# Kernel optimization log

Measured on AMD Instinct MI355X. Metric: run time of the kernel, lower is better.

## Reference

```python
import jax, jax.numpy as jnp
import numpy as np

N_NODES = 100000
N_EDGES = 1600000
IN_F = 512
OUT_F = 128


def setup_inputs() -> dict:
    key = jax.random.key(0)
    k1, k2, k3, k4, k5 = jax.random.split(key, 5)
    x = jax.random.normal(k1, (N_NODES, IN_F), dtype=jnp.float32)
    adj_row = jnp.sort(jax.random.randint(k2, (N_EDGES,), 0, N_NODES, dtype=jnp.int32))
    adj_col = jax.random.randint(k3, (N_EDGES,), 0, N_NODES, dtype=jnp.int32)
    adj_vals = jax.random.uniform(k4, (N_EDGES,), dtype=jnp.float32)
    # Xavier-uniform init like nn.init.xavier_uniform_
    limit = float(np.sqrt(6.0 / (IN_F + OUT_F)))
    weight = jax.random.uniform(k5, (IN_F, OUT_F), minval=-limit, maxval=limit, dtype=jnp.float32)
    return {"x": x, "adj_row": adj_row, "adj_col": adj_col, "adj_vals": adj_vals, "weight": weight}


def reference(x, adj_row, adj_col, adj_vals, weight):
    # support = input @ weight  (dense GEMM; torch.spmm with dense-equivalent input)
    support = x @ weight                      # [N, OUT_F]
    # output = adj @ support, adj in COO: gather cols, scale, segment-sum by row
    msgs = adj_vals[:, None] * support[adj_col]          # [E, OUT_F]
    output = jax.ops.segment_sum(msgs, adj_row, num_segments=N_NODES)  # [N, OUT_F]
    return output
```

## Files before the change

### kernel.cpp

```cpp
#include <hip/hip_runtime.h>
#include <hip/hip_bf16.h>

typedef __bf16 bf16;
typedef __attribute__((ext_vector_type(8))) __bf16 bf16x8;
typedef __attribute__((ext_vector_type(4))) __bf16 bf16x4;
typedef __attribute__((ext_vector_type(2))) __bf16 bf16x2;
typedef __attribute__((ext_vector_type(4))) float f32x4;

#define IN_F 512
#define OUT_F 128
#define BM 64
#define BK 64
#define NKT (IN_F / BK)
#define RPB 32
#define PAGE 512
#define UNR 16

__global__ __launch_bounds__(256) void wt_convert_kernel(const float* __restrict__ w,
                                                         bf16* __restrict__ wt_frag) {
    int o = blockIdx.x * 256 + threadIdx.x;
    int e   = o & 7;
    int l   = (o >> 3) & 63;
    int nb  = (o >> 9) & 7;
    int kkt = o >> 12;
    int n = nb * 16 + (l & 15);
    int k = (kkt >> 1) * 64 + (kkt & 1) * 32 + (l >> 4) * 8 + e;
    wt_frag[o] = (bf16)w[k * OUT_F + n];
}

__global__ __launch_bounds__(256) void row_ptr_kernel(const int* __restrict__ adj_row,
                                                      int* __restrict__ row_ptr,
                                                      int n_edges, int n_nodes) {
    int e = blockIdx.x * 256 + threadIdx.x;
    if (e >= n_edges) return;
    int r1 = adj_row[e];
    int r0 = (e == 0) ? -1 : adj_row[e - 1];
    for (int r = r0 + 1; r <= r1; ++r) row_ptr[r] = e;
    if (e == n_edges - 1)
        for (int r = r1 + 1; r <= n_nodes; ++r) row_ptr[r] = n_edges;
}

__global__ __launch_bounds__(256) void gemm_kernel(const float* __restrict__ x,
                                                   const bf16* __restrict__ wt_frag,
                                                   bf16* __restrict__ support,
                                                   int n_nodes) {
    __shared__ bf16 As[2][BM * BK];

    const int tid  = threadIdx.x;
    const int lane = tid & 63;
    const int wid  = tid >> 6;
    const int row0 = blockIdx.x * BM;

    float4 av[4];

    auto load_tile = [&](int kt) {
        const int k0 = kt * BK;
        #pragma unroll
        for (int i = 0; i < 4; ++i) {
            int li = i * 256 + tid;
            int r = li >> 4, c4 = li & 15;
            int grow = row0 + r;
            float4 v = {0.f, 0.f, 0.f, 0.f};
            if (grow < n_nodes)
                v = *reinterpret_cast<const float4*>(x + (size_t)grow * IN_F + k0 + c4 * 4);
            av[i] = v;
        }
    };

    auto write_tile = [&](int buf) {
        char* Ab = (char*)As[buf];
        #pragma unroll
        for (int i = 0; i < 4; ++i) {
            int li = i * 256 + tid;
            int r = li >> 4, c4 = li & 15;
            bf16x4 b;
            b[0] = (bf16)av[i].x; b[1] = (bf16)av[i].y;
            b[2] = (bf16)av[i].z; b[3] = (bf16)av[i].w;
            *reinterpret_cast<bf16x4*>(Ab + ((r * 128 + c4 * 8) ^ ((r & 7) << 4))) = b;
        }
    };

    load_tile(0);
    write_tile(0);
    __syncthreads();

    f32x4 acc[4][2] = {};

    for (int kt = 0; kt < NKT; ++kt) {
        const int cur = kt & 1;

        bf16x8 b[2][2];
        #pragma unroll
        for (int kk = 0; kk < 2; ++kk)
            #pragma unroll
            for (int n = 0; n < 2; ++n) {
                int f = (kt * 2 + kk) * 8 + (wid * 2 + n);
                b[kk][n] = *reinterpret_cast<const bf16x8*>(wt_frag + ((size_t)f * 64 + lane) * 8);
            }

        if (kt < NKT - 1) load_tile(kt + 1);

        const char* Ab = (const char*)As[cur];
        #pragma unroll
        for (int kk = 0; kk < 2; ++kk) {
            const int kbyte = kk * 64 + (lane >> 4) * 16;
            bf16x8 a[4];
            #pragma unroll
            for (int m = 0; m < 4; ++m) {
                int r = m * 16 + (lane & 15);
                a[m] = *reinterpret_cast<const bf16x8*>(Ab + ((r * 128 + kbyte) ^ ((r & 7) << 4)));
            }
            #pragma unroll
            for (int m = 0; m < 4; ++m)
                #pragma unroll
                for (int n = 0; n < 2; ++n)
                    acc[m][n] = __builtin_amdgcn_mfma_f32_16x16x32_bf16(a[m], b[kk][n], acc[m][n], 0, 0, 0);
        }

        if (kt < NKT - 1) {
            write_tile(cur ^ 1);
            __syncthreads();
        }
    }

    #pragma unroll
    for (int m = 0; m < 4; ++m) {
        #pragma unroll
        for (int n = 0; n < 2; ++n) {
            #pragma unroll
            for (int j = 0; j < 4; ++j) {
                int gm = row0 + m * 16 + (lane >> 4) * 4 + j;
                int gn = wid * 32 + n * 16 + (lane & 15);
                if (gm < n_nodes)
                    support[(size_t)gm * OUT_F + gn] = (bf16)acc[m][n][j];
            }
        }
    }
}

__global__ __launch_bounds__(64) void scatter_kernel(const int* __restrict__ adj_row,
                                                     const int* __restrict__ adj_col,
                                                     const float* __restrict__ adj_vals,
                                                     const bf16* __restrict__ support,
                                                     const int* __restrict__ row_ptr,
                                                     float* __restrict__ out,
                                                     int n_nodes) {
    __shared__ int   srow[PAGE];
    __shared__ int   scol[PAGE];
    __shared__ float sval[PAGE];

    const int t    = threadIdx.x;
    const int r0   = blockIdx.x * RPB;
    const int rEnd = min(r0 + RPB, n_nodes);
    const int eLo  = row_ptr[r0];
    const int eHi  = row_ptr[rEnd];

    float accx = 0.f, accy = 0.f;
    int   cur  = r0;

    auto flush_to = [&](int rNew) {
        if (cur < rEnd) {
            float2 st = {accx, accy};
            *reinterpret_cast<float2*>(out + (size_t)cur * OUT_F + t * 2) = st;
        }
        float2 z = {0.f, 0.f};
        int zhi = rNew < rEnd ? rNew : rEnd;
        for (int r = cur + 1; r < zhi; ++r)
            *reinterpret_cast<float2*>(out + (size_t)r * OUT_F + t * 2) = z;
        accx = 0.f; accy = 0.f;
        cur = rNew;
    };

    for (int base = eLo; base < eHi; base += PAGE) {
        const int nE = min(PAGE, eHi - base);
        __syncthreads();
        for (int i = t; i < nE; i += 64) {
            srow[i] = adj_row[base + i];
            scol[i] = adj_col[base + i];
            sval[i] = adj_vals[base + i];
        }
        __syncthreads();
        if (nE < PAGE) {
            for (int i = nE + t; i < PAGE; i += 64) {
                srow[i] = n_nodes;
                scol[i] = 0;
                sval[i] = 0.f;
            }
            __syncthreads();
        }

        for (int i0 = 0; i0 < PAGE; i0 += UNR) {
            if (i0 >= nE) break;
            float mx[UNR], my[UNR];
            #pragma unroll
            for (int u = 0; u < UNR; ++u) {
                int   c = scol[i0 + u];
                float s = sval[i0 + u];
                bf16x2 v = *reinterpret_cast<const bf16x2*>(support + (size_t)c * OUT_F + t * 2);
                mx[u] = s * (float)v[0];
                my[u] = s * (float)v[1];
            }
            #pragma unroll
            for (int u = 0; u < UNR; ++u) {
                int r = srow[i0 + u];
                if (r != cur) flush_to(r);
                accx += mx[u]; accy += my[u];
            }
        }
    }
    flush_to(rEnd);
}

extern "C" void kernel_launch(void* const* d_in, const int* in_sizes, int n_in,
                              void* d_out, int out_size, void* d_ws, size_t ws_size,
                              hipStream_t stream) {
    const float* x        = (const float*)d_in[0];
    const int*   adj_row  = (const int*)d_in[1];
    const int*   adj_col  = (const int*)d_in[2];
    const float* adj_vals = (const float*)d_in[3];
    const float* weight   = (const float*)d_in[4];
    float*       out      = (float*)d_out;

    const int n_nodes = in_sizes[0] / IN_F;
    const int n_edges = in_sizes[1];

    char* ws = (char*)d_ws;
    bf16* support = (bf16*)ws;
    bf16* wt_frag = (bf16*)(ws + (size_t)n_nodes * OUT_F * 2);
    int*  row_ptr = (int*)(ws + (size_t)n_nodes * OUT_F * 2 + IN_F * OUT_F * 2);

    wt_convert_kernel<<<(IN_F * OUT_F) / 256, 256, 0, stream>>>(weight, wt_frag);

    row_ptr_kernel<<<(n_edges + 255) / 256, 256, 0, stream>>>(adj_row, row_ptr,
                                                              n_edges, n_nodes);

    int gemm_blocks = (n_nodes + BM - 1) / BM;
    gemm_kernel<<<gemm_blocks, 256, 0, stream>>>(x, wt_frag, support, n_nodes);

    int scat_blocks = (n_nodes + RPB - 1) / RPB;
    scatter_kernel<<<scat_blocks, 64, 0, stream>>>(adj_row, adj_col, adj_vals,
                                                   support, row_ptr, out, n_nodes);
}
```

Before: 123.4 us.

## Restructure scatter into per-wave independent row segments with no block syncs

The scatter kernel now runs four independent wavefronts per block, each owning 8 rows with its own shared-memory edge page, instead of one 64-thread block over 32 rows. Because each wave only touches its own staging buffers, the __syncthreads barriers are dropped and padding is limited to the next UNR boundary. The gather loop now loads raw 32-bit words first and defers the scaling to the accumulate step, which lowers register pressure. This is meant to raise occupancy and cut synchronisation, but it relies on wave-level execution ordering for shared-memory visibility without any barrier.

```diff
diff --git a/kernel.cpp b/kernel.cpp
--- a/kernel.cpp
+++ b/kernel.cpp
@@ -12,8 +12,9 @@
 #define BM 64
 #define BK 64
 #define NKT (IN_F / BK)
-#define RPB 32
-#define PAGE 512
+#define RPW 8
+#define WPB 4
+#define PAGE 256
 #define UNR 16
 
 __global__ __launch_bounds__(256) void wt_convert_kernel(const float* __restrict__ w,
@@ -138,20 +139,22 @@
     }
 }
 
-__global__ __launch_bounds__(64) void scatter_kernel(const int* __restrict__ adj_row,
-                                                     const int* __restrict__ adj_col,
-                                                     const float* __restrict__ adj_vals,
-                                                     const bf16* __restrict__ support,
-                                                     const int* __restrict__ row_ptr,
-                                                     float* __restrict__ out,
-                                                     int n_nodes) {
-    __shared__ int   srow[PAGE];
-    __shared__ int   scol[PAGE];
-    __shared__ float sval[PAGE];
-
-    const int t    = threadIdx.x;
-    const int r0   = blockIdx.x * RPB;
-    const int rEnd = min(r0 + RPB, n_nodes);
+__global__ __launch_bounds__(256, 8) void scatter_kernel(const int* __restrict__ adj_row,
+                                                         const int* __restrict__ adj_col,
+                                                         const float* __restrict__ adj_vals,
+                                                         const bf16* __restrict__ support,
+                                                         const int* __restrict__ row_ptr,
+                                                         float* __restrict__ out,
+                                                         int n_nodes) {
+    __shared__ int   srow[WPB][PAGE];
+    __shared__ int   scol[WPB][PAGE];
+    __shared__ float sval[WPB][PAGE];
+
+    const int t  = threadIdx.x & 63;
+    const int w  = threadIdx.x >> 6;
+    const int r0 = blockIdx.x * (WPB * RPW) + w * RPW;
+    if (r0 >= n_nodes) return;
+    const int rEnd = min(r0 + RPW, n_nodes);
     const int eLo  = row_ptr[r0];
     const int eHi  = row_ptr[rEnd];
 
@@ -173,38 +176,36 @@
 
     for (int base = eLo; base < eHi; base += PAGE) {
         const int nE = min(PAGE, eHi - base);
-        __syncthreads();
         for (int i = t; i < nE; i += 64) {
-            srow[i] = adj_row[base + i];
-            scol[i] = adj_col[base + i];
-            sval[i] = adj_vals[base + i];
-        }
-        __syncthreads();
-        if (nE < PAGE) {
-            for (int i = nE + t; i < PAGE; i += 64) {
-                srow[i] = n_nodes;
-                scol[i] = 0;
-                sval[i] = 0.f;
-            }
-            __syncthreads();
-        }
-
-        for (int i0 = 0; i0 < PAGE; i0 += UNR) {
-            if (i0 >= nE) break;
-            float mx[UNR], my[UNR];
-            #pragma unroll
-            for (int u = 0; u < UNR; ++u) {
-                int   c = scol[i0 + u];
-                float s = sval[i0 + u];
-                bf16x2 v = *reinterpret_cast<const bf16x2*>(support + (size_t)c * OUT_F + t * 2);
-                mx[u] = s * (float)v[0];
-                my[u] = s * (float)v[1];
-            }
-            #pragma unroll
-            for (int u = 0; u < UNR; ++u) {
-                int r = srow[i0 + u];
+            srow[w][i] = adj_row[base + i];
+            scol[w][i] = adj_col[base + i];
+            sval[w][i] = adj_vals[base + i];
+        }
+        const int nEpad = (nE + UNR - 1) & ~(UNR - 1);
+        {
+            int i = nE + t;
+            if (i < nEpad) {
+                srow[w][i] = n_nodes;
+                scol[w][i] = 0;
+                sval[w][i] = 0.f;
+            }
+        }
+
+        for (int i0 = 0; i0 < nE; i0 += UNR) {
+            unsigned int u[UNR];
+            #pragma unroll
+            for (int k = 0; k < UNR; ++k) {
+                int c = scol[w][i0 + k];
+                u[k] = *reinterpret_cast<const unsigned int*>(support + (size_t)c * OUT_F + t * 2);
+            }
+            #pragma unroll
+            for (int k = 0; k < UNR; ++k) {
+                int r = srow[w][i0 + k];
                 if (r != cur) flush_to(r);
-                accx += mx[u]; accy += my[u];
+                float  s = sval[w][i0 + k];
+                bf16x2 v = __builtin_bit_cast(bf16x2, u[k]);
+                accx += s * (float)v[0];
+                accy += s * (float)v[1];
             }
         }
     }
@@ -237,7 +238,7 @@
     int gemm_blocks = (n_nodes + BM - 1) / BM;
     gemm_kernel<<<gemm_blocks, 256, 0, stream>>>(x, wt_frag, support, n_nodes);
 
-    int scat_blocks = (n_nodes + RPB - 1) / RPB;
-    scatter_kernel<<<scat_blocks, 64, 0, stream>>>(adj_row, adj_col, adj_vals,
-                                                   support, row_ptr, out, n_nodes);
-}
+    int scat_blocks = (n_nodes + WPB * RPW - 1) / (WPB * RPW);
+    scatter_kernel<<<scat_blocks, WPB * 64, 0, stream>>>(adj_row, adj_col, adj_vals,
+                                                         support, row_ptr, out, n_nodes);
+}
```

Result: no change. 123.4 us (+0.0%).
